# Kernel tuning notes

Measured on AMD Instinct MI355X. Metric: run time of the kernel, lower is better.

Reference implementation:

```python
import jax, jax.numpy as jnp
import numpy as np

D = 64      # in_features
U = 1024    # hidden units
B = 4096    # batch

def _build_masks():
    d0 = np.arange(D)
    dh = np.arange(U) % (D - 1)
    m0 = (d0[None, :] <= dh[:, None]).astype(np.float32)          # [U, D]
    m1 = (dh[None, :] <= dh[:, None]).astype(np.float32)          # [U, U]
    m2 = np.tile((dh[None, :] < d0[:, None]).astype(np.float32), (2, 1))  # [2D, U]
    return jnp.asarray(m0), jnp.asarray(m1), jnp.asarray(m2)


def setup_inputs() -> dict:
    key = jax.random.key(0)
    ks = jax.random.split(key, 7)
    scale = 0.02  # small init so exp(sigma) stays finite
    return {
        "u": jax.random.normal(ks[0], (B, D), dtype=jnp.float32),
        "W0": jax.random.normal(ks[1], (U, D), dtype=jnp.float32) * scale,
        "b0": jax.random.normal(ks[2], (U,), dtype=jnp.float32) * scale,
        "W1": jax.random.normal(ks[3], (U, U), dtype=jnp.float32) * scale,
        "b1": jax.random.normal(ks[4], (U,), dtype=jnp.float32) * scale,
        "W2": jax.random.normal(ks[5], (2 * D, U), dtype=jnp.float32) * scale,
        "b2": jax.random.normal(ks[6], (2 * D,), dtype=jnp.float32) * scale,
    }


def reference(u, W0, b0, W1, b1, W2, b2):
    m0, m1, m2 = _build_masks()
    mW0, mW1, mW2 = m0 * W0, m1 * W1, m2 * W2  # masked weights (constant across steps)

    def made(x):  # x: [B, D] -> mu, sigma each [B, D]
        h = jax.nn.relu(x @ mW0.T + b0)
        h = jax.nn.relu(h @ mW1.T + b1)
        z = h @ mW2.T + b2
        return z[:, :D], z[:, D:]

    def step(carry, i):
        x, ldj = carry
        mu, sigma = made(x)
        # ordering = arange(D) (sequential, not reversed) => idx == i
        x = x.at[:, i].set(u[:, i] * jnp.exp(sigma[:, i]) + mu[:, i])
        ldj = ldj.at[:, i].set(sigma[:, i])
        return (x, ldj), None

    x0 = jnp.zeros_like(u)
    ldj0 = jnp.zeros_like(u)
    (x, ldj), _ = jax.lax.scan(step, (x0, ldj0), jnp.arange(D))
    log_det_jacobian = jnp.sum(ldj, axis=1, keepdims=True)  # [B, 1]
    return x, log_det_jacobian
```

## Files before the change

kernel.cpp:

```cpp
#include <hip/hip_runtime.h>
#include <hip/hip_bf16.h>

#define BATCH 4096
#define NTHR 512

typedef __attribute__((ext_vector_type(8))) short bf16x8;
typedef __attribute__((ext_vector_type(4))) float f32x4;
typedef __attribute__((ext_vector_type(4))) short short4v;

#define BAR() asm volatile("s_waitcnt lgkmcnt(0)\n\ts_barrier" ::: "memory")

__host__ __device__ __forceinline__ int off1(int g) { return (g <= 16) ? 17 * g : 16 * g + 16; }
__host__ __device__ __forceinline__ int cntg(int g) { return (g < 16) ? 17 : 16; }
__host__ __device__ __forceinline__ int unitOf(int p) {
    int gp, jp;
    if (p < 272) { gp = p / 17; jp = p - gp * 17; }
    else         { gp = (p >> 4) - 1; jp = p & 15; }
    return gp + 63 * jp;
}
__device__ __forceinline__ short f2bf(float f) {
    __hip_bfloat16 h = __float2bfloat16(f);
    return *reinterpret_cast<short*>(&h);
}

__global__ void prep6(const float* __restrict__ W0, const float* __restrict__ b0,
                      const float* __restrict__ W1, const float* __restrict__ b1,
                      const float* __restrict__ W2,
                      short* __restrict__ W1f, short* __restrict__ W2f,
                      short* __restrict__ W0f, float* __restrict__ b1p) {
    __shared__ short ws[16][1024];
    const int b = blockIdx.x, t = threadIdx.x;
    if (b < 72) {
        const bool isW1 = (b < 64);
        const int n = t >> 5;
        int u;
        if (isW1) u = unitOf(b * 16 + n);
        else { const int c = b - 64; u = (n & 1) ? (64 + c * 8 + (n >> 1)) : (c * 8 + (n >> 1)); }
        const float* src = isW1 ? (W1 + (long)u * 1024) : (W2 + (long)u * 1024);
        const int c0 = (t & 31) * 4;
#pragma unroll
        for (int j = 0; j < 8; ++j) {
            int c = c0 + j * 128;
            float4 v = *(const float4*)&src[c];
            short4v sv;
            sv[0] = f2bf(v.x); sv[1] = f2bf(v.y); sv[2] = f2bf(v.z); sv[3] = f2bf(v.w);
            *(short4v*)&ws[n][c] = sv;
        }
        __syncthreads();
#pragma unroll 1
        for (int it = 0; it < 8; ++it) {
            int v = t + it * 512;
            if (v < 4032) {
                int g = v >> 6, lane2 = v & 63;
                int nn = lane2 & 15, aq2 = lane2 >> 4;
                bf16x8 pk;
#pragma unroll
                for (int e = 0; e < 8; ++e) {
                    int k = aq2 * 8 + e;
                    pk[e] = (k < cntg(g)) ? ws[nn][g + 63 * k] : (short)0;
                }
                if (isW1) *(bf16x8*)&W1f[(((long)g * 64 + b) * 64 + lane2) * 8] = pk;
                else      *(bf16x8*)&W2f[(((long)g * 8 + (b - 64)) * 64 + lane2) * 8] = pk;
            }
        }
    } else if (b < 88) {
        const int bb = b - 72;
#pragma unroll 1
        for (int j = 0; j < 16; ++j) {
            int q = t + j * 512;
            if (q < 8064) {
                int idx = bb * 8064 + q;
                int g = idx >> 11, rem = idx & 2047;
                int n2 = rem >> 10, kt = (rem >> 9) & 1, lane2 = (rem >> 3) & 63, e = rem & 7;
                int sl = n2 * 16 + (lane2 & 15);
                int kp = kt * 32 + ((lane2 >> 4) << 3) + e;
                float val = 0.f;
                if (sl < cntg(g)) {
                    int u = unitOf(off1(g) + sl);
                    if (kp == 0) val = b0[u];
                    else if (kp - 1 <= g) val = W0[u * 64 + kp - 1];
                }
                W0f[idx] = f2bf(val);
            }
        }
    } else {
        for (int p = t; p < 1024; p += 512) b1p[p] = b1[unitOf(p)];
    }
}

__global__ __launch_bounds__(NTHR, 2) void made6(
    const float* __restrict__ uin, const float* __restrict__ b2,
    const short* __restrict__ W1f, const short* __restrict__ W2f,
    const short* __restrict__ W0f, const float* __restrict__ b1p,
    float* __restrict__ out) {

    __shared__ __align__(16) short h1g[16][40];
    __shared__ __align__(16) short h2g[16][40];
    __shared__ __align__(16) short xhist[16][80];
    __shared__ __align__(16) float uT[64][16];
    __shared__ __align__(16) float xLs[16][68];
    __shared__ float ldjpart[8][16];

    const int t = threadIdx.x, lane = t & 63, wv = t >> 6;
    const int n = lane & 15, aq = lane >> 4;
    const int rowbase = blockIdx.x * 16;

    {
        int* z1 = (int*)&h1g[0][0];
        for (int idx = t; idx < 16 * 40 / 2; idx += NTHR) z1[idx] = 0;
        int* z2 = (int*)&h2g[0][0];
        for (int idx = t; idx < 16 * 40 / 2; idx += NTHR) z2[idx] = 0;
        int* z3 = (int*)&xhist[0][0];
        for (int idx = t; idx < 16 * 80 / 2; idx += NTHR) z3[idx] = 0;
    }
    if (t < 256) {
        int r = t >> 4, c0 = (t & 15) * 4;
        float4 v = *(const float4*)&uin[(long)(rowbase + r) * 64 + c0];
        uT[c0 + 0][r] = v.x; uT[c0 + 1][r] = v.y; uT[c0 + 2][r] = v.z; uT[c0 + 3][r] = v.w;
    }

    f32x4 acc2[8];
#pragma unroll
    for (int s = 0; s < 8; ++s) {
        float bb = b1p[(wv + 8 * s) * 16 + n];
        acc2[s] = (f32x4){bb, bb, bb, bb};
    }
    f32x4 zacc;
    {
        int pc = wv * 16 + n;
        float bz = b2[(pc >> 1) + 64 * (pc & 1)];
        zacc = (f32x4){bz, bz, bz, bz};
    }

    bf16x8 w1fE[8], w1fO[8], w2fE, w2fO, w0f0, w0f1, w0f2;
#pragma unroll
    for (int s = 0; s < 8; ++s) {
        const int tile = wv + 8 * s;
        w1fO[s] = *(const bf16x8*)&W1f[(((long)0 * 64 + tile) * 64 + lane) * 8];
        w1fE[s] = *(const bf16x8*)&W1f[(((long)1 * 64 + tile) * 64 + lane) * 8];
    }
    w2fO = *(const bf16x8*)&W2f[(((long)0 * 8 + wv) * 64 + lane) * 8];
    w2fE = *(const bf16x8*)&W2f[(((long)1 * 8 + wv) * 64 + lane) * 8];
    {
        const long gb = 8 * wv;
        w0f0 = *(const bf16x8*)&W0f[((gb * 4 + 0) * 64 + lane) * 8];
        w0f1 = *(const bf16x8*)&W0f[((gb * 4 + 1) * 64 + lane) * 8];
        w0f2 = *(const bf16x8*)&W0f[((gb * 4 + 2) * 64 + lane) * 8];
    }

    f32x4 ldjacc = {0.f, 0.f, 0.f, 0.f};
    BAR();
    if (t < 16) xhist[t][0] = (short)0x3F80;
    float ureg[4];
#pragma unroll
    for (int r = 0; r < 4; ++r) ureg[r] = uT[8 * wv + (n >> 1)][aq * 4 + r];

    auto body = [&](int i, bf16x8* w1fS, bf16x8& w2fS) {
        const int g = i - 1;
        if (g >= 0) {
            const int og = off1(g), cg = cntg(g);
            const int tf0 = og >> 4, tfl = (og + cg - 1) >> 4;
            const int s0 = (tf0 > wv) ? ((tf0 - wv + 7) >> 3) : 0;
            if (s0 < 8) {
                const bf16x8 af = *(const bf16x8*)&h1g[n][aq * 8];
#pragma unroll
                for (int s = 0; s < 8; ++s)
                    if (s >= s0)
                        acc2[s] = __builtin_amdgcn_mfma_f32_16x16x32_bf16(af, w1fS[s], acc2[s], 0, 0, 0);
            }
            {
                const int gp = (i + 1 < 63) ? (i + 1) : 62;
                const int tf0p = off1(gp) >> 4;
                const int s0p = (tf0p > wv) ? ((tf0p - wv + 7) >> 3) : 0;
#pragma unroll
                for (int s = 0; s < 8; ++s)
                    if (s >= s0p)
                        w1fS[s] = *(const bf16x8*)&W1f[(((long)gp * 64 + (wv + 8 * s)) * 64 + lane) * 8];
            }
            if (wv == (tf0 & 7)) {
                const int sT = tf0 >> 3;
                const int j = tf0 * 16 + n - og;
                if (j >= 0 && j < cg) {
#pragma unroll
                    for (int r = 0; r < 4; ++r) {
                        float v = acc2[sT][r];
                        h2g[aq * 4 + r][j] = f2bf(v > 0.f ? v : 0.f);
                    }
                }
            }
            if (tfl != tf0 && wv == (tfl & 7)) {
                const int sT = tfl >> 3;
                const int j = tfl * 16 + n - og;
                if (j < cg) {
#pragma unroll
                    for (int r = 0; r < 4; ++r) {
                        float v = acc2[sT][r];
                        h2g[aq * 4 + r][j] = f2bf(v > 0.f ? v : 0.f);
                    }
                }
            }
            if (g == 16 && wv == 0 && n == 0) {
#pragma unroll
                for (int r = 0; r < 4; ++r) h2g[aq * 4 + r][16] = 0;
            }
        }
        BAR();
        if (g >= 0) {
            const bf16x8 af3 = *(const bf16x8*)&h2g[n][aq * 8];
            zacc = __builtin_amdgcn_mfma_f32_16x16x32_bf16(af3, w2fS, zacc, 0, 0, 0);
            const int gp = (i + 1 < 63) ? (i + 1) : 62;
            w2fS = *(const bf16x8*)&W2f[(((long)gp * 8 + wv) * 64 + lane) * 8];
        }
        if (wv == (i >> 3)) {
            const int n0 = 2 * (i & 7);
            f32x4 sgv;
#pragma unroll
            for (int r = 0; r < 4; ++r) sgv[r] = __shfl_xor(zacc[r], 1);
            if (n == n0) {
#pragma unroll
                for (int r = 0; r < 4; ++r) {
                    const float sg = sgv[r], mu = zacc[r];
                    const float x = ureg[r] * __expf(sg) + mu;
                    ldjacc[r] += sg;
                    const int m = aq * 4 + r;
                    xLs[m][i] = x;
                    if (i < 63) xhist[m][i + 1] = f2bf(x);
                }
            }
            if (i < 63) {
                const bf16x8 ax0 = *(const bf16x8*)&xhist[n][aq * 8];
                f32x4 d0 = {0.f, 0.f, 0.f, 0.f};
                d0 = __builtin_amdgcn_mfma_f32_16x16x32_bf16(ax0, w0f0, d0, 0, 0, 0);
                if (i >= 31) {
                    const bf16x8 ax1 = *(const bf16x8*)&xhist[n][32 + aq * 8];
                    d0 = __builtin_amdgcn_mfma_f32_16x16x32_bf16(ax1, w0f1, d0, 0, 0, 0);
                }
                f32x4 d1 = {0.f, 0.f, 0.f, 0.f};
                if (i < 16)
                    d1 = __builtin_amdgcn_mfma_f32_16x16x32_bf16(ax0, w0f2, d1, 0, 0, 0);
#pragma unroll
                for (int r = 0; r < 4; ++r) {
                    float v = d0[r];
                    h1g[aq * 4 + r][n] = f2bf(v > 0.f ? v : 0.f);
                }
                if (n == 0) {
#pragma unroll
                    for (int r = 0; r < 4; ++r) {
                        float v = (i < 16) ? (d1[r] > 0.f ? d1[r] : 0.f) : 0.f;
                        h1g[aq * 4 + r][16] = f2bf(v);
                    }
                }
                if (i + 1 < 63 && ((i + 1) >> 3) == wv) {
                    const long gb = i + 1;
                    w0f0 = *(const bf16x8*)&W0f[((gb * 4 + 0) * 64 + lane) * 8];
                    w0f1 = *(const bf16x8*)&W0f[((gb * 4 + 1) * 64 + lane) * 8];
                    w0f2 = *(const bf16x8*)&W0f[((gb * 4 + 2) * 64 + lane) * 8];
                }
            }
        }
        BAR();
    };

#pragma unroll 1
    for (int i = 0; i < 64; i += 2) {
        body(i, w1fE, w2fE);
        body(i + 1, w1fO, w2fO);
    }

#pragma unroll
    for (int r = 0; r < 4; ++r) {
        float v = ldjacc[r];
        v += __shfl_xor(v, 2);
        v += __shfl_xor(v, 4);
        v += __shfl_xor(v, 8);
        if (n == 0) ldjpart[wv][aq * 4 + r] = v;
    }
    BAR();

    if (t < 256) {
        int r = t >> 4, c = (t & 15) * 4;
        float4 v;
        v.x = xLs[r][c]; v.y = xLs[r][c + 1]; v.z = xLs[r][c + 2]; v.w = xLs[r][c + 3];
        *(float4*)&out[(long)(rowbase + r) * 64 + c] = v;
    }
    if (t < 16) {
        float s = 0.f;
#pragma unroll
        for (int w = 0; w < 8; ++w) s += ldjpart[w][t];
        out[(long)BATCH * 64 + rowbase + t] = s;
    }
}

extern "C" void kernel_launch(void* const* d_in, const int* in_sizes, int n_in,
                              void* d_out, int out_size, void* d_ws, size_t ws_size,
                              hipStream_t stream) {
    (void)in_sizes; (void)n_in; (void)out_size; (void)ws_size;
    const float* u  = (const float*)d_in[0];
    const float* W0 = (const float*)d_in[1];
    const float* b0 = (const float*)d_in[2];
    const float* W1 = (const float*)d_in[3];
    const float* b1 = (const float*)d_in[4];
    const float* W2 = (const float*)d_in[5];
    const float* b2 = (const float*)d_in[6];
    float* out = (float*)d_out;

    short* W1f = (short*)d_ws;
    short* W2f = (short*)((char*)d_ws + 4128768);
    short* W0f = (short*)((char*)d_ws + 4128768 + 516096);
    float* b1p = (float*)((char*)d_ws + 4128768 + 516096 + 258048);

    prep6<<<dim3(89), dim3(512), 0, stream>>>(W0, b0, W1, b1, W2, W1f, W2f, W0f, b1p);
    made6<<<dim3(BATCH / 16), dim3(NTHR), 0, stream>>>(u, b2, W1f, W2f, W0f, b1p, out);
}
```

Before: 177.5 us.

## Run eight sequential steps per wave with deferred catch-up, cutting barriers per step

The 64-step sequential loop is restructured so that one wave at a time owns a block of 8 consecutive steps. It computes those steps alone, without block-wide barriers between them. Other waves later catch up on the hidden-layer-2 and output contributions in a batched pass, using double-buffered per-step h1/h2 staging in shared memory. The new-x contribution to h1 is applied as a scalar fused update (x times the diagonal W0 entry) rather than waiting on the xhist write. The aim is to cut per-step barrier and latency cost on the serial critical path. The cost is that the serial phases leave the other waves idle, and it adds more LDS and register pressure plus redundant W1 fragment loads.

```diff
diff --git a/kernel.cpp b/kernel.cpp
--- a/kernel.cpp
+++ b/kernel.cpp
@@ -9,6 +9,7 @@
 typedef __attribute__((ext_vector_type(4))) short short4v;
 
 #define BAR() asm volatile("s_waitcnt lgkmcnt(0)\n\ts_barrier" ::: "memory")
+#define MFMA16(a, b, c) __builtin_amdgcn_mfma_f32_16x16x32_bf16(a, b, c, 0, 0, 0)
 
 __host__ __device__ __forceinline__ int off1(int g) { return (g <= 16) ? 17 * g : 16 * g + 16; }
 __host__ __device__ __forceinline__ int cntg(int g) { return (g < 16) ? 17 : 16; }
@@ -21,6 +22,10 @@
 __device__ __forceinline__ short f2bf(float f) {
     __hip_bfloat16 h = __float2bfloat16(f);
     return *reinterpret_cast<short*>(&h);
+}
+__device__ __forceinline__ float bfrnd(float f) {
+    __hip_bfloat16 h = __float2bfloat16(f);
+    return __bfloat162float(h);
 }
 
 __global__ void prep6(const float* __restrict__ W0, const float* __restrict__ b0,
@@ -88,14 +93,15 @@
     }
 }
 
-__global__ __launch_bounds__(NTHR, 2) void made6(
+__global__ __launch_bounds__(NTHR, 2) void made7(
     const float* __restrict__ uin, const float* __restrict__ b2,
+    const float* __restrict__ W0,
     const short* __restrict__ W1f, const short* __restrict__ W2f,
     const short* __restrict__ W0f, const float* __restrict__ b1p,
     float* __restrict__ out) {
 
-    __shared__ __align__(16) short h1g[16][40];
-    __shared__ __align__(16) short h2g[16][40];
+    __shared__ __align__(16) short h1w[2][8][16][40];
+    __shared__ __align__(16) short h2w[2][8][16][40];
     __shared__ __align__(16) short xhist[16][80];
     __shared__ __align__(16) float uT[64][16];
     __shared__ __align__(16) float xLs[16][68];
@@ -106,12 +112,15 @@
     const int rowbase = blockIdx.x * 16;
 
     {
-        int* z1 = (int*)&h1g[0][0];
-        for (int idx = t; idx < 16 * 40 / 2; idx += NTHR) z1[idx] = 0;
-        int* z2 = (int*)&h2g[0][0];
-        for (int idx = t; idx < 16 * 40 / 2; idx += NTHR) z2[idx] = 0;
+        int* z1 = (int*)&h1w[0][0][0][0];
+#pragma unroll 1
+        for (int idx = t; idx < 5120; idx += NTHR) z1[idx] = 0;
+        int* z2 = (int*)&h2w[0][0][0][0];
+#pragma unroll 1
+        for (int idx = t; idx < 5120; idx += NTHR) z2[idx] = 0;
         int* z3 = (int*)&xhist[0][0];
-        for (int idx = t; idx < 16 * 80 / 2; idx += NTHR) z3[idx] = 0;
+#pragma unroll 1
+        for (int idx = t; idx < 640; idx += NTHR) z3[idx] = 0;
     }
     if (t < 256) {
         int r = t >> 4, c0 = (t & 15) * 4;
@@ -119,11 +128,16 @@
         uT[c0 + 0][r] = v.x; uT[c0 + 1][r] = v.y; uT[c0 + 2][r] = v.z; uT[c0 + 3][r] = v.w;
     }
 
-    f32x4 acc2[8];
-#pragma unroll
-    for (int s = 0; s < 8; ++s) {
-        float bb = b1p[(wv + 8 * s) * 16 + n];
-        acc2[s] = (f32x4){bb, bb, bb, bb};
+    const int gA = (wv == 0) ? 0 : 8 * wv - 1;
+    const int gB = (8 * wv + 6 > 62) ? 62 : 8 * wv + 6;
+    const int TLO = off1(gA) >> 4;
+    const int NT = ((off1(gB) + cntg(gB) - 1) >> 4) - TLO + 1;
+
+    f32x4 acc2own[9];
+#pragma unroll
+    for (int tt = 0; tt < 9; ++tt) {
+        float bb = (tt < NT) ? b1p[(TLO + tt) * 16 + n] : 0.f;
+        acc2own[tt] = (f32x4){bb, bb, bb, bb};
     }
     f32x4 zacc;
     {
@@ -132,150 +146,196 @@
         zacc = (f32x4){bz, bz, bz, bz};
     }
 
-    bf16x8 w1fE[8], w1fO[8], w2fE, w2fO, w0f0, w0f1, w0f2;
-#pragma unroll
-    for (int s = 0; s < 8; ++s) {
-        const int tile = wv + 8 * s;
-        w1fO[s] = *(const bf16x8*)&W1f[(((long)0 * 64 + tile) * 64 + lane) * 8];
-        w1fE[s] = *(const bf16x8*)&W1f[(((long)1 * 64 + tile) * 64 + lane) * 8];
-    }
-    w2fO = *(const bf16x8*)&W2f[(((long)0 * 8 + wv) * 64 + lane) * 8];
-    w2fE = *(const bf16x8*)&W2f[(((long)1 * 8 + wv) * 64 + lane) * 8];
-    {
-        const long gb = 8 * wv;
-        w0f0 = *(const bf16x8*)&W0f[((gb * 4 + 0) * 64 + lane) * 8];
-        w0f1 = *(const bf16x8*)&W0f[((gb * 4 + 1) * 64 + lane) * 8];
-        w0f2 = *(const bf16x8*)&W0f[((gb * 4 + 2) * 64 + lane) * 8];
+    float w0d[8], w0d16[8];
+#pragma unroll
+    for (int k = 0; k < 8; ++k) {
+        const int i = 8 * wv + k;
+        float v = 0.f, v16 = 0.f;
+        if (i < 63) {
+            v = bfrnd(W0[unitOf(off1(i) + n) * 64 + i]);
+            if (i < 16) v16 = bfrnd(W0[unitOf(off1(i) + 16) * 64 + i]);
+        }
+        w0d[k] = v; w0d16[k] = v16;
     }
 
     f32x4 ldjacc = {0.f, 0.f, 0.f, 0.f};
+    bf16x8 w1A[9], w1B[9], w2E, w2O, w0fa, w0fb, w0fc;
+
     BAR();
     if (t < 16) xhist[t][0] = (short)0x3F80;
     float ureg[4];
 #pragma unroll
     for (int r = 0; r < 4; ++r) ureg[r] = uT[8 * wv + (n >> 1)][aq * 4 + r];
 
-    auto body = [&](int i, bf16x8* w1fS, bf16x8& w2fS) {
-        const int g = i - 1;
+    auto catchup = [&](int w) {
+#pragma unroll
+        for (int gk = 0; gk < 8; ++gk) {
+            const int g = 8 * w - 9 + gk;
+            if (g >= 0) {
+                bf16x8 a3 = *(const bf16x8*)&h2w[(g >> 3) & 1][g & 7][n][aq * 8];
+                bf16x8 wb = *(const bf16x8*)&W2f[(((long)g * 8 + wv) * 64 + lane) * 8];
+                zacc = MFMA16(a3, wb, zacc);
+            }
+        }
+        const int pH = (w - 1) & 1;
+        const long g0 = 8 * (w - 1);
+#pragma unroll
+        for (int tt = 0; tt < 9; ++tt)
+            if (tt < NT) w1A[tt] = *(const bf16x8*)&W1f[(((g0 + 0) * 64 + TLO + tt) * 64 + lane) * 8];
+#pragma unroll 1
+        for (int gk = 0; gk < 8; gk += 2) {
+#pragma unroll
+            for (int tt = 0; tt < 9; ++tt)
+                if (tt < NT) w1B[tt] = *(const bf16x8*)&W1f[(((g0 + gk + 1) * 64 + TLO + tt) * 64 + lane) * 8];
+            {
+                bf16x8 af = *(const bf16x8*)&h1w[pH][gk][n][aq * 8];
+#pragma unroll
+                for (int tt = 0; tt < 9; ++tt)
+                    if (tt < NT) acc2own[tt] = MFMA16(af, w1A[tt], acc2own[tt]);
+            }
+            if (gk + 2 < 8) {
+#pragma unroll
+                for (int tt = 0; tt < 9; ++tt)
+                    if (tt < NT) w1A[tt] = *(const bf16x8*)&W1f[(((g0 + gk + 2) * 64 + TLO + tt) * 64 + lane) * 8];
+            }
+            {
+                bf16x8 af = *(const bf16x8*)&h1w[pH][gk + 1][n][aq * 8];
+#pragma unroll
+                for (int tt = 0; tt < 9; ++tt)
+                    if (tt < NT) acc2own[tt] = MFMA16(af, w1B[tt], acc2own[tt]);
+            }
+        }
+    };
+
+    auto step = [&](int wq, int k, bf16x8 (&wApply)[9], bf16x8 (&wLoad)[9], bf16x8& w2S) {
+        const int i = 8 * wq + k, g = i - 1;
+        if (k > 0) {
+            const int t0g = (off1(g) >> 4) - TLO;
+            bf16x8 af = *(const bf16x8*)&h1w[(g >> 3) & 1][g & 7][n][aq * 8];
+#pragma unroll
+            for (int tt = 0; tt < 9; ++tt)
+                if (tt < NT && tt >= t0g) acc2own[tt] = MFMA16(af, wApply[tt], acc2own[tt]);
+        }
+        if (k < 7) {
+            const long gl = i;
+#pragma unroll
+            for (int tt = 0; tt < 9; ++tt)
+                if (tt < NT) wLoad[tt] = *(const bf16x8*)&W1f[((gl * 64 + TLO + tt) * 64 + lane) * 8];
+        }
         if (g >= 0) {
             const int og = off1(g), cg = cntg(g);
-            const int tf0 = og >> 4, tfl = (og + cg - 1) >> 4;
-            const int s0 = (tf0 > wv) ? ((tf0 - wv + 7) >> 3) : 0;
-            if (s0 < 8) {
-                const bf16x8 af = *(const bf16x8*)&h1g[n][aq * 8];
-#pragma unroll
-                for (int s = 0; s < 8; ++s)
-                    if (s >= s0)
-                        acc2[s] = __builtin_amdgcn_mfma_f32_16x16x32_bf16(af, w1fS[s], acc2[s], 0, 0, 0);
-            }
-            {
-                const int gp = (i + 1 < 63) ? (i + 1) : 62;
-                const int tf0p = off1(gp) >> 4;
-                const int s0p = (tf0p > wv) ? ((tf0p - wv + 7) >> 3) : 0;
-#pragma unroll
-                for (int s = 0; s < 8; ++s)
-                    if (s >= s0p)
-                        w1fS[s] = *(const bf16x8*)&W1f[(((long)gp * 64 + (wv + 8 * s)) * 64 + lane) * 8];
-            }
-            if (wv == (tf0 & 7)) {
-                const int sT = tf0 >> 3;
-                const int j = tf0 * 16 + n - og;
-                if (j >= 0 && j < cg) {
+            const int tf0 = (og >> 4) - TLO, tfl = ((og + cg - 1) >> 4) - TLO;
+            const int p2 = (g >> 3) & 1, s2 = g & 7;
+            const int j0 = (tf0 + TLO) * 16 + n - og;
+            const int j1 = (tfl + TLO) * 16 + n - og;
+#pragma unroll
+            for (int tt = 0; tt < 9; ++tt) {
+                if (tt == tf0 && j0 >= 0 && j0 < cg) {
 #pragma unroll
                     for (int r = 0; r < 4; ++r) {
-                        float v = acc2[sT][r];
-                        h2g[aq * 4 + r][j] = f2bf(v > 0.f ? v : 0.f);
+                        float v = acc2own[tt][r];
+                        h2w[p2][s2][aq * 4 + r][j0] = f2bf(v > 0.f ? v : 0.f);
                     }
                 }
-            }
-            if (tfl != tf0 && wv == (tfl & 7)) {
-                const int sT = tfl >> 3;
-                const int j = tfl * 16 + n - og;
-                if (j < cg) {
+                if (tfl != tf0 && tt == tfl && j1 < cg) {
 #pragma unroll
                     for (int r = 0; r < 4; ++r) {
-                        float v = acc2[sT][r];
-                        h2g[aq * 4 + r][j] = f2bf(v > 0.f ? v : 0.f);
+                        float v = acc2own[tt][r];
+                        h2w[p2][s2][aq * 4 + r][j1] = f2bf(v > 0.f ? v : 0.f);
                     }
                 }
             }
-            if (g == 16 && wv == 0 && n == 0) {
-#pragma unroll
-                for (int r = 0; r < 4; ++r) h2g[aq * 4 + r][16] = 0;
-            }
+            if (cg == 16 && n == 0) {
+#pragma unroll
+                for (int r = 0; r < 4; ++r) h2w[p2][s2][aq * 4 + r][16] = 0;
+            }
+        }
+        f32x4 d0p = {0.f, 0.f, 0.f, 0.f}, d1p = {0.f, 0.f, 0.f, 0.f};
+        const bool doH1 = (i < 63);
+        if (doH1) {
+            bf16x8 ax0 = *(const bf16x8*)&xhist[n][aq * 8];
+            d0p = MFMA16(ax0, w0fa, d0p);
+            if (i >= 32) {
+                bf16x8 ax1 = *(const bf16x8*)&xhist[n][32 + aq * 8];
+                d0p = MFMA16(ax1, w0fb, d0p);
+            }
+            if (i < 16) d1p = MFMA16(ax0, w0fc, d1p);
+        }
+        if (g >= 0) {
+            bf16x8 af3 = *(const bf16x8*)&h2w[(g >> 3) & 1][g & 7][n][aq * 8];
+            zacc = MFMA16(af3, w2S, zacc);
+        }
+        if (k < 7) {
+            const long gp = (i + 1 < 63) ? i + 1 : 62;
+            w2S = *(const bf16x8*)&W2f[((gp * 8 + wv) * 64 + lane) * 8];
+        }
+        const int n0 = 2 * k;
+        f32x4 sgv;
+#pragma unroll
+        for (int r = 0; r < 4; ++r) sgv[r] = __shfl_xor(zacc[r], 1);
+        float xv[4];
+        if (n == n0) {
+#pragma unroll
+            for (int r = 0; r < 4; ++r) {
+                const float sg = sgv[r], mu = zacc[r];
+                const float x = ureg[r] * __expf(sg) + mu;
+                ldjacc[r] += sg;
+                xv[r] = x;
+                xLs[aq * 4 + r][i] = x;
+                if (doH1) xhist[aq * 4 + r][i + 1] = f2bf(x);
+            }
+        }
+        if (doH1) {
+            const int pi = (i >> 3) & 1, si = i & 7;
+#pragma unroll
+            for (int r = 0; r < 4; ++r) {
+                float xb = bfrnd(__shfl(xv[r], (lane & 48) | n0));
+                float h = d0p[r] + xb * w0d[k];
+                h1w[pi][si][aq * 4 + r][n] = f2bf(h > 0.f ? h : 0.f);
+                if (n == 0) {
+                    float h16 = (i < 16) ? (d1p[r] + xb * w0d16[k]) : 0.f;
+                    h1w[pi][si][aq * 4 + r][16] = f2bf(h16 > 0.f ? h16 : 0.f);
+                }
+            }
+            if (k < 7) {
+                const long gb = i + 1;
+                w0fa = *(const bf16x8*)&W0f[((gb * 4 + 0) * 64 + lane) * 8];
+                w0fb = *(const bf16x8*)&W0f[((gb * 4 + 1) * 64 + lane) * 8];
+                w0fc = *(const bf16x8*)&W0f[((gb * 4 + 2) * 64 + lane) * 8];
+            }
+        }
+    };
+
+#pragma unroll 1
+    for (int w = 0; w < 8; ++w) {
+        if (wv == w) {
+            __builtin_amdgcn_s_setprio(1);
+            const long i0 = 8 * w;
+            if (w > 0) w2E = *(const bf16x8*)&W2f[(((i0 - 1) * 8 + wv) * 64 + lane) * 8];
+            w2O = *(const bf16x8*)&W2f[((i0 * 8 + wv) * 64 + lane) * 8];
+            w0fa = *(const bf16x8*)&W0f[((i0 * 4 + 0) * 64 + lane) * 8];
+            w0fb = *(const bf16x8*)&W0f[((i0 * 4 + 1) * 64 + lane) * 8];
+            w0fc = *(const bf16x8*)&W0f[((i0 * 4 + 2) * 64 + lane) * 8];
+            if (w > 0) catchup(w);
+#pragma unroll
+            for (int k = 0; k < 8; k += 2) {
+                step(w, k,     w1B, w1A, w2E);
+                step(w, k + 1, w1A, w1B, w2O);
+            }
+#pragma unroll
+            for (int r = 0; r < 4; ++r) {
+                float v = ldjacc[r];
+                v += __shfl_xor(v, 2);
+                v += __shfl_xor(v, 4);
+                v += __shfl_xor(v, 8);
+                if (n == 0) ldjpart[wv][aq * 4 + r] = v;
+            }
+            __builtin_amdgcn_s_setprio(0);
+        } else if (w > 0 && wv > w) {
+            catchup(w);
         }
         BAR();
-        if (g >= 0) {
-            const bf16x8 af3 = *(const bf16x8*)&h2g[n][aq * 8];
-            zacc = __builtin_amdgcn_mfma_f32_16x16x32_bf16(af3, w2fS, zacc, 0, 0, 0);
-            const int gp = (i + 1 < 63) ? (i + 1) : 62;
-            w2fS = *(const bf16x8*)&W2f[(((long)gp * 8 + wv) * 64 + lane) * 8];
-        }
-        if (wv == (i >> 3)) {
-            const int n0 = 2 * (i & 7);
-            f32x4 sgv;
-#pragma unroll
-            for (int r = 0; r < 4; ++r) sgv[r] = __shfl_xor(zacc[r], 1);
-            if (n == n0) {
-#pragma unroll
-                for (int r = 0; r < 4; ++r) {
-                    const float sg = sgv[r], mu = zacc[r];
-                    const float x = ureg[r] * __expf(sg) + mu;
-                    ldjacc[r] += sg;
-                    const int m = aq * 4 + r;
-                    xLs[m][i] = x;
-                    if (i < 63) xhist[m][i + 1] = f2bf(x);
-                }
-            }
-            if (i < 63) {
-                const bf16x8 ax0 = *(const bf16x8*)&xhist[n][aq * 8];
-                f32x4 d0 = {0.f, 0.f, 0.f, 0.f};
-                d0 = __builtin_amdgcn_mfma_f32_16x16x32_bf16(ax0, w0f0, d0, 0, 0, 0);
-                if (i >= 31) {
-                    const bf16x8 ax1 = *(const bf16x8*)&xhist[n][32 + aq * 8];
-                    d0 = __builtin_amdgcn_mfma_f32_16x16x32_bf16(ax1, w0f1, d0, 0, 0, 0);
-                }
-                f32x4 d1 = {0.f, 0.f, 0.f, 0.f};
-                if (i < 16)
-                    d1 = __builtin_amdgcn_mfma_f32_16x16x32_bf16(ax0, w0f2, d1, 0, 0, 0);
-#pragma unroll
-                for (int r = 0; r < 4; ++r) {
-                    float v = d0[r];
-                    h1g[aq * 4 + r][n] = f2bf(v > 0.f ? v : 0.f);
-                }
-                if (n == 0) {
-#pragma unroll
-                    for (int r = 0; r < 4; ++r) {
-                        float v = (i < 16) ? (d1[r] > 0.f ? d1[r] : 0.f) : 0.f;
-                        h1g[aq * 4 + r][16] = f2bf(v);
-                    }
-                }
-                if (i + 1 < 63 && ((i + 1) >> 3) == wv) {
-                    const long gb = i + 1;
-                    w0f0 = *(const bf16x8*)&W0f[((gb * 4 + 0) * 64 + lane) * 8];
-                    w0f1 = *(const bf16x8*)&W0f[((gb * 4 + 1) * 64 + lane) * 8];
-                    w0f2 = *(const bf16x8*)&W0f[((gb * 4 + 2) * 64 + lane) * 8];
-                }
-            }
-        }
-        BAR();
-    };
-
-#pragma unroll 1
-    for (int i = 0; i < 64; i += 2) {
-        body(i, w1fE, w2fE);
-        body(i + 1, w1fO, w2fO);
-    }
-
-#pragma unroll
-    for (int r = 0; r < 4; ++r) {
-        float v = ldjacc[r];
-        v += __shfl_xor(v, 2);
-        v += __shfl_xor(v, 4);
-        v += __shfl_xor(v, 8);
-        if (n == 0) ldjpart[wv][aq * 4 + r] = v;
-    }
-    BAR();
+    }
 
     if (t < 256) {
         int r = t >> 4, c = (t & 15) * 4;
@@ -286,7 +346,7 @@
     if (t < 16) {
         float s = 0.f;
 #pragma unroll
-        for (int w = 0; w < 8; ++w) s += ldjpart[w][t];
+        for (int w2 = 0; w2 < 8; ++w2) s += ldjpart[w2][t];
         out[(long)BATCH * 64 + rowbase + t] = s;
     }
 }
@@ -310,5 +370,5 @@
     float* b1p = (float*)((char*)d_ws + 4128768 + 516096 + 258048);
 
     prep6<<<dim3(89), dim3(512), 0, stream>>>(W0, b0, W1, b1, W2, W1f, W2f, W0f, b1p);
-    made6<<<dim3(BATCH / 16), dim3(NTHR), 0, stream>>>(u, b2, W1f, W2f, W0f, b1p, out);
-}
+    made7<<<dim3(BATCH / 16), dim3(NTHR), 0, stream>>>(u, b2, W0, W1f, W2f, W0f, b1p, out);
+}
```

After: 421.1 us. +137.2%, slower.

## Hoist layer-0 MFMA off the serial x dependency with a rank-1 correction

Applied to the files above, without the earlier changes.

In the serial per-column step, the layer-0 MFMA now runs on the x history before the new x_i is computed. The contribution of x_i is then added afterwards as a scalar rank-1 correction, using a prefetched bf16-rounded W0 column. This takes the MFMA latency off the exp/shuffle critical path, and the active wave gets raised scheduling priority through s_setprio. In exchange it adds per-step global loads of W0 entries and an extra shuffle, and it relies on the not-yet-written xhist slot being zero.

```diff
diff --git a/kernel.cpp b/kernel.cpp
--- a/kernel.cpp
+++ b/kernel.cpp
@@ -21,6 +21,10 @@
 __device__ __forceinline__ short f2bf(float f) {
     __hip_bfloat16 h = __float2bfloat16(f);
     return *reinterpret_cast<short*>(&h);
+}
+__device__ __forceinline__ float bfrnd(float f) {
+    __hip_bfloat16 h = __float2bfloat16(f);
+    return __bfloat162float(h);
 }
 
 __global__ void prep6(const float* __restrict__ W0, const float* __restrict__ b0,
@@ -88,8 +92,9 @@
     }
 }
 
-__global__ __launch_bounds__(NTHR, 2) void made6(
+__global__ __launch_bounds__(NTHR, 2) void made9(
     const float* __restrict__ uin, const float* __restrict__ b2,
+    const float* __restrict__ W0,
     const short* __restrict__ W1f, const short* __restrict__ W2f,
     const short* __restrict__ W0f, const float* __restrict__ b1p,
     float* __restrict__ out) {
@@ -146,6 +151,12 @@
         w0f0 = *(const bf16x8*)&W0f[((gb * 4 + 0) * 64 + lane) * 8];
         w0f1 = *(const bf16x8*)&W0f[((gb * 4 + 1) * 64 + lane) * 8];
         w0f2 = *(const bf16x8*)&W0f[((gb * 4 + 2) * 64 + lane) * 8];
+    }
+    float w0dCur, w0d16Cur;
+    {
+        const int i0 = 8 * wv;
+        w0dCur = bfrnd(W0[unitOf(off1(i0) + n) * 64 + i0]);
+        w0d16Cur = (i0 < 16) ? bfrnd(W0[unitOf(off1(i0) + 16) * 64 + i0]) : 0.f;
     }
 
     f32x4 ldjacc = {0.f, 0.f, 0.f, 0.f};
@@ -212,42 +223,52 @@
             w2fS = *(const bf16x8*)&W2f[(((long)gp * 8 + wv) * 64 + lane) * 8];
         }
         if (wv == (i >> 3)) {
+            __builtin_amdgcn_s_setprio(1);
             const int n0 = 2 * (i & 7);
+            const bool doH1 = (i < 63);
+            f32x4 d0p = {0.f, 0.f, 0.f, 0.f}, d1p = {0.f, 0.f, 0.f, 0.f};
+            if (doH1) {
+                const bf16x8 ax0 = *(const bf16x8*)&xhist[n][aq * 8];
+                d0p = __builtin_amdgcn_mfma_f32_16x16x32_bf16(ax0, w0f0, d0p, 0, 0, 0);
+                if (i >= 31) {
+                    const bf16x8 ax1 = *(const bf16x8*)&xhist[n][32 + aq * 8];
+                    d0p = __builtin_amdgcn_mfma_f32_16x16x32_bf16(ax1, w0f1, d0p, 0, 0, 0);
+                }
+                if (i < 16)
+                    d1p = __builtin_amdgcn_mfma_f32_16x16x32_bf16(ax0, w0f2, d1p, 0, 0, 0);
+            }
             f32x4 sgv;
 #pragma unroll
             for (int r = 0; r < 4; ++r) sgv[r] = __shfl_xor(zacc[r], 1);
+            f32x4 xv;
             if (n == n0) {
 #pragma unroll
                 for (int r = 0; r < 4; ++r) {
                     const float sg = sgv[r], mu = zacc[r];
                     const float x = ureg[r] * __expf(sg) + mu;
                     ldjacc[r] += sg;
+                    xv[r] = x;
                     const int m = aq * 4 + r;
                     xLs[m][i] = x;
-                    if (i < 63) xhist[m][i + 1] = f2bf(x);
-                }
-            }
-            if (i < 63) {
-                const bf16x8 ax0 = *(const bf16x8*)&xhist[n][aq * 8];
-                f32x4 d0 = {0.f, 0.f, 0.f, 0.f};
-                d0 = __builtin_amdgcn_mfma_f32_16x16x32_bf16(ax0, w0f0, d0, 0, 0, 0);
-                if (i >= 31) {
-                    const bf16x8 ax1 = *(const bf16x8*)&xhist[n][32 + aq * 8];
-                    d0 = __builtin_amdgcn_mfma_f32_16x16x32_bf16(ax1, w0f1, d0, 0, 0, 0);
-                }
-                f32x4 d1 = {0.f, 0.f, 0.f, 0.f};
-                if (i < 16)
-                    d1 = __builtin_amdgcn_mfma_f32_16x16x32_bf16(ax0, w0f2, d1, 0, 0, 0);
+                    if (doH1) xhist[m][i + 1] = f2bf(x);
+                }
+            }
+            if (doH1) {
 #pragma unroll
                 for (int r = 0; r < 4; ++r) {
-                    float v = d0[r];
-                    h1g[aq * 4 + r][n] = f2bf(v > 0.f ? v : 0.f);
-                }
-                if (n == 0) {
-#pragma unroll
-                    for (int r = 0; r < 4; ++r) {
-                        float v = (i < 16) ? (d1[r] > 0.f ? d1[r] : 0.f) : 0.f;
-                        h1g[aq * 4 + r][16] = f2bf(v);
+                    const float xb = bfrnd(__shfl(xv[r], (lane & 48) | n0));
+                    const float h = d0p[r] + xb * w0dCur;
+                    h1g[aq * 4 + r][n] = f2bf(h > 0.f ? h : 0.f);
+                    if (n == 0) {
+                        const float h16 = (i < 16) ? (d1p[r] + xb * w0d16Cur) : 0.f;
+                        h1g[aq * 4 + r][16] = f2bf(h16 > 0.f ? h16 : 0.f);
+                    }
+                }
+                if ((i & 7) < 7) {
+                    const int i2 = i + 1;
+                    if (i2 < 63) {
+                        w0dCur = bfrnd(W0[unitOf(off1(i2) + n) * 64 + i2]);
+                        w0d16Cur = (i2 < 16) ? bfrnd(W0[unitOf(off1(i2) + 16) * 64 + i2]) : 0.f;
                     }
                 }
                 if (i + 1 < 63 && ((i + 1) >> 3) == wv) {
@@ -257,6 +278,7 @@
                     w0f2 = *(const bf16x8*)&W0f[((gb * 4 + 2) * 64 + lane) * 8];
                 }
             }
+            __builtin_amdgcn_s_setprio(0);
         }
         BAR();
     };
@@ -310,5 +332,5 @@
     float* b1p = (float*)((char*)d_ws + 4128768 + 516096 + 258048);
 
     prep6<<<dim3(89), dim3(512), 0, stream>>>(W0, b0, W1, b1, W2, W1f, W2f, W0f, b1p);
-    made6<<<dim3(BATCH / 16), dim3(NTHR), 0, stream>>>(u, b2, W1f, W2f, W0f, b1p, out);
-}
+    made9<<<dim3(BATCH / 16), dim3(NTHR), 0, stream>>>(u, b2, W0, W1f, W2f, W0f, b1p, out);
+}
```

Measured after the change: 215.8 us. 1.22x slower.
